# Kernel tuning notes

Hardware: AMD Instinct MI355X
Metric: run time of the kernel (lower is better)

Reference implementation:

```python
import jax, jax.numpy as jnp
import numpy as np

B, T, N, E = 8, 16, 2048, 32768
F_IN, C, EDGE_DIM = 32, 32, 1


def setup_inputs() -> dict:
    key = jax.random.key(0)
    ks = jax.random.split(key, 12)
    s = 1.0 / np.sqrt(C)
    x = jax.random.normal(ks[0], (B, T, N, F_IN), jnp.float32)
    edge_index = jax.random.randint(ks[1], (2, E), 0, N)
    edge_attr = jax.random.normal(ks[2], (E, EDGE_DIM), jnp.float32)
    Wl = jax.random.normal(ks[3], (F_IN, C), jnp.float32) * s
    bl = jnp.zeros((C,), jnp.float32)
    Wr = jax.random.normal(ks[4], (F_IN, C), jnp.float32) * s
    br = jnp.zeros((C,), jnp.float32)
    We = jax.random.normal(ks[5], (EDGE_DIM, C), jnp.float32) * s
    att = jax.random.normal(ks[6], (C,), jnp.float32) * s
    out_bias = jnp.zeros((C,), jnp.float32)
    w_ih = jax.random.normal(ks[7], (3 * C, C), jnp.float32) * s
    w_hh = jax.random.normal(ks[8], (3 * C, C), jnp.float32) * s
    b_ih = jnp.zeros((3 * C,), jnp.float32)
    b_hh = jnp.zeros((3 * C,), jnp.float32)
    return dict(x=x, edge_index=edge_index, edge_attr=edge_attr, Wl=Wl, bl=bl,
                Wr=Wr, br=br, We=We, att=att, out_bias=out_bias,
                w_ih=w_ih, w_hh=w_hh, b_ih=b_ih, b_hh=b_hh)


def _gatv2(x, edge_index, edge_attr, Wl, bl, Wr, br, We, att, out_bias):
    # x: [B,T,N,F]; GATv2Conv, heads=1, negative_slope=0.2, self loops w/ mean edge attr
    n = x.shape[2]
    src, dst = edge_index[0], edge_index[1]
    deg = jax.ops.segment_sum(jnp.ones((src.shape[0],), x.dtype), dst, num_segments=n)
    mean_attr = jax.ops.segment_sum(edge_attr, dst, num_segments=n) / jnp.maximum(deg, 1.0)[:, None]
    loop = jnp.arange(n)
    src_a = jnp.concatenate([src, loop])
    dst_a = jnp.concatenate([dst, loop])
    attr_a = jnp.concatenate([edge_attr, mean_attr], axis=0)
    xl = x @ Wl + bl  # [B,T,N,C]
    xr = x @ Wr + br
    e_emb = attr_a @ We  # [E2,C]
    xls = jnp.take(xl, src_a, axis=2)  # [B,T,E2,C]
    m = jax.nn.leaky_relu(xls + jnp.take(xr, dst_a, axis=2) + e_emb, 0.2)
    s = jnp.einsum('btec,c->ebt', m, att)  # [E2,B,T]
    smax = jax.ops.segment_max(s, dst_a, num_segments=n)
    es = jnp.exp(s - smax[dst_a])
    denom = jax.ops.segment_sum(es, dst_a, num_segments=n)
    alpha = es / denom[dst_a]  # segment softmax over incoming edges, [E2,B,T]
    msg = xls * alpha.transpose(1, 2, 0)[..., None]  # [B,T,E2,C]
    out = jax.ops.segment_sum(msg.transpose(2, 0, 1, 3), dst_a, num_segments=n)
    return out.transpose(1, 2, 0, 3) + out_bias  # [B,T,N,C]


def _gru(seq, w_ih, w_hh, b_ih, b_hh):
    # seq: [BN, T, C]; torch GRU gate order r,z,n
    c = seq.shape[-1]

    def step(h, xt):
        gi = xt @ w_ih.T + b_ih
        gh = h @ w_hh.T + b_hh
        ir, iz, inn = jnp.split(gi, 3, axis=-1)
        hr, hz, hn = jnp.split(gh, 3, axis=-1)
        r = jax.nn.sigmoid(ir + hr)
        z = jax.nn.sigmoid(iz + hz)
        nc = jnp.tanh(inn + r * hn)
        h = (1.0 - z) * nc + z * h
        return h, h

    h0 = jnp.zeros((seq.shape[0], c), seq.dtype)
    _, ys = jax.lax.scan(step, h0, seq.transpose(1, 0, 2))
    return ys.transpose(1, 0, 2)


def reference(x, edge_index, edge_attr, Wl, bl, Wr, br, We, att, out_bias, w_ih, w_hh, b_ih, b_hh):
    b, t, n, _ = x.shape
    h = _gatv2(x, edge_index, edge_attr, Wl, bl, Wr, br, We, att, out_bias)
    seq = h.transpose(0, 2, 1, 3).reshape(b * n, t, -1)
    y = _gru(seq, w_ih, w_hh, b_ih, b_hh)
    return y.reshape(b, n, t, -1).transpose(0, 2, 1, 3)
```

## Files before the change

kernel.cpp:

```cpp
#include <hip/hip_runtime.h>
#include <hip/hip_bf16.h>

#define N_NODES 2048
#define N_EDGES 32768
#define BT      128
#define TT      16
#define CH      32
#define E2      (N_EDGES + N_NODES)

static __device__ __forceinline__ unsigned pk2(float a, float b) {
    __hip_bfloat162 h2(__float2bfloat16(a), __float2bfloat16(b));
    return *reinterpret_cast<unsigned*>(&h2);
}

__global__ void deg_attr_kernel(const int* __restrict__ ei,
                                const float* __restrict__ ea,
                                int* __restrict__ deg, float* __restrict__ asum) {
    int e = blockIdx.x * 256 + threadIdx.x;
    if (e < N_EDGES) {
        int dst = ei[N_EDGES + e];
        atomicAdd(&deg[dst], 1);
        atomicAdd(&asum[dst], ea[e]);
    }
}

__global__ void scan_kernel(const int* __restrict__ deg, int* __restrict__ rowp) {
    int lane = threadIdx.x;
    int base = lane * 32;
    int loc[32];
    int s = 0;
    #pragma unroll
    for (int i = 0; i < 32; ++i) { loc[i] = s; s += deg[base + i] + 1; }
    int inc = s;
    #pragma unroll
    for (int d = 1; d < 64; d <<= 1) {
        int v = __shfl_up(inc, d, 64);
        if (lane >= d) inc += v;
    }
    int excl = inc - s;
    #pragma unroll
    for (int i = 0; i < 32; ++i) rowp[base + i] = excl + loc[i];
    if (lane == 63) rowp[N_NODES] = inc;
}

__global__ void scatter_kernel(const int* __restrict__ ei,
                               const float* __restrict__ ea,
                               const int* __restrict__ deg, const float* __restrict__ asum,
                               const int* __restrict__ rowp, int* __restrict__ fill,
                               int* __restrict__ col, float* __restrict__ attr_s) {
    int e = blockIdx.x * 256 + threadIdx.x;
    if (e >= E2) return;
    int src, dst; float a;
    if (e < N_EDGES) {
        src = ei[e]; dst = ei[N_EDGES + e]; a = ea[e];
    } else {
        int n = e - N_EDGES;
        src = n; dst = n;
        a = asum[n] / fmaxf((float)deg[n], 1.0f);
    }
    int pos = atomicAdd(&fill[dst], 1);
    col[rowp[dst] + pos]    = src;
    attr_s[rowp[dst] + pos] = a;
}

__global__ __launch_bounds__(256) void proj_kernel(
        const float* __restrict__ x,
        const float* __restrict__ Wl, const float* __restrict__ bl,
        unsigned* __restrict__ xlt) {
    __shared__ float xs[128 * 32];
    __shared__ float wl[1024];
    int n = blockIdx.x;
    int tid = threadIdx.x;
    for (int i = tid; i < 1024; i += 256) wl[i] = Wl[i];
    #pragma unroll
    for (int i = 0; i < 16; ++i) {
        int e = i * 256 + tid;
        int bt = e >> 5, f = e & 31;
        xs[e] = x[((long)bt * N_NODES + n) * 32 + f];
    }
    __syncthreads();
    int c2  = tid & 15;
    int btl = tid >> 4;
    int c0 = 2 * c2, c1 = c0 + 1;
    float b0 = bl[c0], b1 = bl[c1];
    for (int i = 0; i < 8; ++i) {
        int bt = i * 16 + btl;
        float a0 = 0.f, a1 = 0.f;
        #pragma unroll
        for (int f = 0; f < 32; ++f) {
            float xv = xs[bt * 32 + f];
            a0 = fmaf(xv, wl[f * 32 + c0], a0);
            a1 = fmaf(xv, wl[f * 32 + c1], a1);
        }
        xlt[((long)n * 16 + c2) * 128 + bt] = pk2(a0 + b0, a1 + b1);
    }
}

__global__ __launch_bounds__(256) void gat_kernel(
        const unsigned* __restrict__ xlt,
        const float* __restrict__ x,
        const int* __restrict__ rowp, const int* __restrict__ col,
        const float* __restrict__ attr_s,
        const float* __restrict__ Wr, const float* __restrict__ br,
        const float* __restrict__ We, const float* __restrict__ att,
        const float* __restrict__ ob,
        const float* __restrict__ wih, const float* __restrict__ bih,
        __hip_bfloat16* __restrict__ gi) {
    int tid = threadIdx.x;
    int wv = tid >> 6, lane = tid & 63;
    int task = blockIdx.x * 4 + wv;
    int n   = task >> 1;
    int bt  = ((task & 1) << 6) | lane;

    float xf[32];
    {
        const float* xp = x + ((long)bt * N_NODES + n) * 32;
        #pragma unroll
        for (int f4 = 0; f4 < 8; ++f4) {
            float4 a = *(const float4*)(xp + f4 * 4);
            xf[f4*4+0]=a.x; xf[f4*4+1]=a.y; xf[f4*4+2]=a.z; xf[f4*4+3]=a.w;
        }
    }
    float xrv[32];
    #pragma unroll
    for (int c = 0; c < 32; ++c) {
        float s = br[c];
        #pragma unroll
        for (int f = 0; f < 32; ++f) s = fmaf(xf[f], Wr[f * 32 + c], s);
        xrv[c] = s;
    }

    float accv[32];
    #pragma unroll
    for (int c = 0; c < 32; ++c) accv[c] = 0.f;

    int beg = rowp[n];
    int end = rowp[n + 1];
    float den = 0.f;
    const unsigned* xbase = xlt + bt;

    unsigned up[16];
    float avp = attr_s[beg];
    {
        const unsigned* gp = xbase + (long)col[beg] * (16 * 128);
        #pragma unroll
        for (int c2 = 0; c2 < 16; ++c2) up[c2] = gp[c2 * 128];
    }

    for (int j = beg; j < end; ++j) {
        int jn = (j + 1 < end) ? (j + 1) : j;
        float avn = attr_s[jn];
        unsigned un[16];
        {
            const unsigned* gp = xbase + (long)col[jn] * (16 * 128);
            #pragma unroll
            for (int c2 = 0; c2 < 16; ++c2) un[c2] = gp[c2 * 128];
        }

        float av = avp;
        float p0 = 0.f, p1 = 0.f, p2 = 0.f, p3 = 0.f;
        #pragma unroll
        for (int c2 = 0; c2 < 16; ++c2) {
            unsigned u = up[c2];
            float x0 = __uint_as_float(u << 16);
            float x1 = __uint_as_float(u & 0xffff0000u);
            int c = 2 * c2;
            float m0 = x0 + fmaf(av, We[c],     xrv[c]);
            float m1 = x1 + fmaf(av, We[c + 1], xrv[c + 1]);
            if (c2 & 1) { p2 = fmaf(att[c], fmaxf(m0, 0.2f * m0), p2);
                          p3 = fmaf(att[c + 1], fmaxf(m1, 0.2f * m1), p3); }
            else        { p0 = fmaf(att[c], fmaxf(m0, 0.2f * m0), p0);
                          p1 = fmaf(att[c + 1], fmaxf(m1, 0.2f * m1), p1); }
        }
        float p = fminf((p0 + p1) + (p2 + p3), 80.f);
        float w = __expf(p);
        den += w;
        #pragma unroll
        for (int c2 = 0; c2 < 16; ++c2) {
            unsigned u = up[c2];
            accv[2*c2]   = fmaf(w, __uint_as_float(u << 16),         accv[2*c2]);
            accv[2*c2+1] = fmaf(w, __uint_as_float(u & 0xffff0000u), accv[2*c2+1]);
        }
        #pragma unroll
        for (int c2 = 0; c2 < 16; ++c2) up[c2] = un[c2];
        avp = avn;
    }
    float inv = 1.f / den;
    #pragma unroll
    for (int c = 0; c < 32; ++c) accv[c] = fmaf(accv[c], inv, ob[c]);

    __hip_bfloat16* gip = gi + ((long)bt * N_NODES + n) * 96;
    #pragma unroll
    for (int g8 = 0; g8 < 12; ++g8) {
        float s0 = bih[g8*8+0], s1 = bih[g8*8+1], s2 = bih[g8*8+2], s3 = bih[g8*8+3];
        float s4 = bih[g8*8+4], s5 = bih[g8*8+5], s6 = bih[g8*8+6], s7 = bih[g8*8+7];
        #pragma unroll
        for (int f = 0; f < 32; ++f) {
            float hf = accv[f];
            s0 = fmaf(hf, wih[(g8*8+0)*32+f], s0);
            s1 = fmaf(hf, wih[(g8*8+1)*32+f], s1);
            s2 = fmaf(hf, wih[(g8*8+2)*32+f], s2);
            s3 = fmaf(hf, wih[(g8*8+3)*32+f], s3);
            s4 = fmaf(hf, wih[(g8*8+4)*32+f], s4);
            s5 = fmaf(hf, wih[(g8*8+5)*32+f], s5);
            s6 = fmaf(hf, wih[(g8*8+6)*32+f], s6);
            s7 = fmaf(hf, wih[(g8*8+7)*32+f], s7);
        }
        uint4 v;
        v.x = pk2(s0, s1); v.y = pk2(s2, s3); v.z = pk2(s4, s5); v.w = pk2(s6, s7);
        *(uint4*)(gip + g8 * 8) = v;
    }
}

__global__ __launch_bounds__(256) void gru_kernel(
        const float* __restrict__ whh, const float* __restrict__ bhh,
        const __hip_bfloat16* __restrict__ gi,
        float* __restrict__ out) {
    int tid  = threadIdx.x;
    int lane = tid & 63;
    int c    = lane & 31;
    int half = lane >> 5;
    int fbase = half << 4;
    int seq  = blockIdx.x * 4 + (tid >> 6);
    int b = seq >> 11;
    int n = seq & 2047;

    float w0[16], w1[16], w2[16];
    #pragma unroll
    for (int k4 = 0; k4 < 4; ++k4) {
        float4 a0 = *(const float4*)&whh[( 0 + c) * 32 + fbase + k4 * 4];
        float4 a1 = *(const float4*)&whh[(32 + c) * 32 + fbase + k4 * 4];
        float4 a2 = *(const float4*)&whh[(64 + c) * 32 + fbase + k4 * 4];
        w0[k4*4+0]=a0.x; w0[k4*4+1]=a0.y; w0[k4*4+2]=a0.z; w0[k4*4+3]=a0.w;
        w1[k4*4+0]=a1.x; w1[k4*4+1]=a1.y; w1[k4*4+2]=a1.z; w1[k4*4+3]=a1.w;
        w2[k4*4+0]=a2.x; w2[k4*4+1]=a2.y; w2[k4*4+2]=a2.z; w2[k4*4+3]=a2.w;
    }
    float bh0 = half ? 0.f : bhh[c];
    float bh1 = half ? 0.f : bhh[32 + c];
    float bh2 = half ? 0.f : bhh[64 + c];

    const long GSTR = (long)N_NODES * 96;
    long gbase = ((long)b * TT * N_NODES + n) * 96 + c;
    const long OSTR = (long)N_NODES * CH;
    long obase = ((long)b * TT * N_NODES + n) * CH + c;

    float hc = 0.f;
    float gr = __bfloat162float(gi[gbase]);
    float gz = __bfloat162float(gi[gbase + 32]);
    float gn = __bfloat162float(gi[gbase + 64]);
    #pragma unroll 1
    for (int t = 0; t < TT; ++t) {
        long gnx = gbase + (long)(t + 1) * GSTR;
        float grn = 0.f, gzn = 0.f, gnn = 0.f;
        if (t + 1 < TT) {
            grn = __bfloat162float(gi[gnx]);
            gzn = __bfloat162float(gi[gnx + 32]);
            gnn = __bfloat162float(gi[gnx + 64]);
        }
        float g0 = bh0, g1 = bh1, g2 = bh2;
        #pragma unroll
        for (int k = 0; k < 16; ++k) {
            float v = __shfl(hc, fbase + k, 64);
            g0 = fmaf(v, w0[k], g0);
            g1 = fmaf(v, w1[k], g1);
            g2 = fmaf(v, w2[k], g2);
        }
        float G0 = g0 + __shfl_xor(g0, 32, 64);
        float G1 = g1 + __shfl_xor(g1, 32, 64);
        float G2 = g2 + __shfl_xor(g2, 32, 64);
        float r  = 1.f / (1.f + __expf(-(gr + G0)));
        float z  = 1.f / (1.f + __expf(-(gz + G1)));
        float a  = fmaf(r, G2, gn);
        float e2 = __expf(2.f * a);
        float nc = 1.f - 2.f / (e2 + 1.f);
        hc = (1.f - z) * nc + z * hc;
        if (half == 0) out[obase + (long)t * OSTR] = hc;
        gr = grn; gz = gzn; gn = gnn;
    }
}

extern "C" void kernel_launch(void* const* d_in, const int* in_sizes, int n_in,
                              void* d_out, int out_size, void* d_ws, size_t ws_size,
                              hipStream_t stream) {
    const float* x    = (const float*)d_in[0];
    const int*   ei   = (const int*)d_in[1];
    const float* ea   = (const float*)d_in[2];
    const float* Wl   = (const float*)d_in[3];
    const float* bl   = (const float*)d_in[4];
    const float* Wr   = (const float*)d_in[5];
    const float* br   = (const float*)d_in[6];
    const float* We   = (const float*)d_in[7];
    const float* att  = (const float*)d_in[8];
    const float* ob   = (const float*)d_in[9];
    const float* wih  = (const float*)d_in[10];
    const float* whh  = (const float*)d_in[11];
    const float* bih  = (const float*)d_in[12];
    const float* bhh  = (const float*)d_in[13];
    float* out = (float*)d_out;

    int*   deg  = (int*)d_ws;
    float* asum = (float*)(deg + N_NODES);
    int*   fill = (int*)(asum + N_NODES);
    int*   rowp = fill + N_NODES;
    int*   col  = rowp + (N_NODES + 16);
    float* attr_s = (float*)(col + E2);
    unsigned* xlt = (unsigned*)(attr_s + E2);
    xlt = (unsigned*)(((uintptr_t)xlt + 255) & ~(uintptr_t)255);
    __hip_bfloat16* gi = (__hip_bfloat16*)(xlt + (long)N_NODES * 16 * 128);

    hipMemsetAsync(deg, 0, 3 * N_NODES * sizeof(int), stream);

    deg_attr_kernel<<<N_EDGES / 256, 256, 0, stream>>>(ei, ea, deg, asum);
    scan_kernel<<<1, 64, 0, stream>>>(deg, rowp);
    scatter_kernel<<<(E2 + 255) / 256, 256, 0, stream>>>(ei, ea, deg, asum, rowp, fill, col, attr_s);
    proj_kernel<<<N_NODES, 256, 0, stream>>>(x, Wl, bl, xlt);
    gat_kernel<<<(N_NODES * 2) / 4, 256, 0, stream>>>(xlt, x, rowp, col, attr_s,
                                                      Wr, br, We, att, ob, wih, bih, gi);
    gru_kernel<<<(BT / TT * N_NODES) / 4, 256, 0, stream>>>(whh, bhh, gi, out);
}
```

Before: 231.6 us.

## Transpose xl layout to channel-contiguous, stage weights in LDS, deepen gather prefetch

```diff
diff --git a/kernel.cpp b/kernel.cpp
--- a/kernel.cpp
+++ b/kernel.cpp
@@ -92,7 +92,7 @@
             a0 = fmaf(xv, wl[f * 32 + c0], a0);
             a1 = fmaf(xv, wl[f * 32 + c1], a1);
         }
-        xlt[((long)n * 16 + c2) * 128 + bt] = pk2(a0 + b0, a1 + b1);
+        xlt[((long)n * 128 + bt) * 16 + c2] = pk2(a0 + b0, a1 + b1);
     }
 }
 
@@ -106,7 +106,13 @@
         const float* __restrict__ ob,
         const float* __restrict__ wih, const float* __restrict__ bih,
         __hip_bfloat16* __restrict__ gi) {
+    __shared__ float wr_s[1024];
+    __shared__ float wi_s[3072];
     int tid = threadIdx.x;
+    for (int i = tid; i < 1024; i += 256) wr_s[i] = Wr[i];
+    for (int i = tid; i < 3072; i += 256) wi_s[i] = wih[i];
+    __syncthreads();
+
     int wv = tid >> 6, lane = tid & 63;
     int task = blockIdx.x * 4 + wv;
     int n   = task >> 1;
@@ -126,7 +132,7 @@
     for (int c = 0; c < 32; ++c) {
         float s = br[c];
         #pragma unroll
-        for (int f = 0; f < 32; ++f) s = fmaf(xf[f], Wr[f * 32 + c], s);
+        for (int f = 0; f < 32; ++f) s = fmaf(xf[f], wr_s[f * 32 + c], s);
         xrv[c] = s;
     }
 
@@ -137,27 +143,32 @@
     int beg = rowp[n];
     int end = rowp[n + 1];
     float den = 0.f;
-    const unsigned* xbase = xlt + bt;
 
     unsigned up[16];
-    float avp = attr_s[beg];
+    float av_j;
+    int src1; float av1;
     {
-        const unsigned* gp = xbase + (long)col[beg] * (16 * 128);
-        #pragma unroll
-        for (int c2 = 0; c2 < 16; ++c2) up[c2] = gp[c2 * 128];
+        int s0 = col[beg]; av_j = attr_s[beg];
+        const uint4* gp = (const uint4*)(xlt + ((long)s0 * 128 + bt) * 16);
+        uint4 a = gp[0], b = gp[1], c = gp[2], d = gp[3];
+        up[0]=a.x; up[1]=a.y; up[2]=a.z;  up[3]=a.w;
+        up[4]=b.x; up[5]=b.y; up[6]=b.z;  up[7]=b.w;
+        up[8]=c.x; up[9]=c.y; up[10]=c.z; up[11]=c.w;
+        up[12]=d.x; up[13]=d.y; up[14]=d.z; up[15]=d.w;
+        int j1 = (beg + 1 < end) ? beg + 1 : beg;
+        src1 = col[j1]; av1 = attr_s[j1];
     }
 
     for (int j = beg; j < end; ++j) {
-        int jn = (j + 1 < end) ? (j + 1) : j;
-        float avn = attr_s[jn];
-        unsigned un[16];
+        uint4 a, b, c4, d;
         {
-            const unsigned* gp = xbase + (long)col[jn] * (16 * 128);
-            #pragma unroll
-            for (int c2 = 0; c2 < 16; ++c2) un[c2] = gp[c2 * 128];
-        }
-
-        float av = avp;
+            const uint4* gp = (const uint4*)(xlt + ((long)src1 * 128 + bt) * 16);
+            a = gp[0]; b = gp[1]; c4 = gp[2]; d = gp[3];
+        }
+        int j2 = (j + 2 < end) ? j + 2 : end - 1;
+        int src2 = col[j2]; float av2 = attr_s[j2];
+
+        float av = av_j;
         float p0 = 0.f, p1 = 0.f, p2 = 0.f, p3 = 0.f;
         #pragma unroll
         for (int c2 = 0; c2 < 16; ++c2) {
@@ -181,9 +192,11 @@
             accv[2*c2]   = fmaf(w, __uint_as_float(u << 16),         accv[2*c2]);
             accv[2*c2+1] = fmaf(w, __uint_as_float(u & 0xffff0000u), accv[2*c2+1]);
         }
-        #pragma unroll
-        for (int c2 = 0; c2 < 16; ++c2) up[c2] = un[c2];
-        avp = avn;
+        up[0]=a.x; up[1]=a.y; up[2]=a.z;  up[3]=a.w;
+        up[4]=b.x; up[5]=b.y; up[6]=b.z;  up[7]=b.w;
+        up[8]=c4.x; up[9]=c4.y; up[10]=c4.z; up[11]=c4.w;
+        up[12]=d.x; up[13]=d.y; up[14]=d.z; up[15]=d.w;
+        av_j = av1; src1 = src2; av1 = av2;
     }
     float inv = 1.f / den;
     #pragma unroll
@@ -197,14 +210,14 @@
         #pragma unroll
         for (int f = 0; f < 32; ++f) {
             float hf = accv[f];
-            s0 = fmaf(hf, wih[(g8*8+0)*32+f], s0);
-            s1 = fmaf(hf, wih[(g8*8+1)*32+f], s1);
-            s2 = fmaf(hf, wih[(g8*8+2)*32+f], s2);
-            s3 = fmaf(hf, wih[(g8*8+3)*32+f], s3);
-            s4 = fmaf(hf, wih[(g8*8+4)*32+f], s4);
-            s5 = fmaf(hf, wih[(g8*8+5)*32+f], s5);
-            s6 = fmaf(hf, wih[(g8*8+6)*32+f], s6);
-            s7 = fmaf(hf, wih[(g8*8+7)*32+f], s7);
+            s0 = fmaf(hf, wi_s[(g8*8+0)*32+f], s0);
+            s1 = fmaf(hf, wi_s[(g8*8+1)*32+f], s1);
+            s2 = fmaf(hf, wi_s[(g8*8+2)*32+f], s2);
+            s3 = fmaf(hf, wi_s[(g8*8+3)*32+f], s3);
+            s4 = fmaf(hf, wi_s[(g8*8+4)*32+f], s4);
+            s5 = fmaf(hf, wi_s[(g8*8+5)*32+f], s5);
+            s6 = fmaf(hf, wi_s[(g8*8+6)*32+f], s6);
+            s7 = fmaf(hf, wi_s[(g8*8+7)*32+f], s7);
         }
         uint4 v;
         v.x = pk2(s0, s1); v.y = pk2(s2, s3); v.z = pk2(s4, s5); v.w = pk2(s6, s7);
```

New measurement: 231.7 us. About the same (+0.0%).
